# Optimization experiments

Measured on AMD Instinct MI355X. Metric: run time of the kernel, lower is better.

Reference implementation:

```python
import jax, jax.numpy as jnp
import numpy as np

NUM_HEADS = 4
NUM_GROUPS = 8
EPS = 1e-5


def group_norm(x, w, b):
    # x: [N, C, H, W], normalize over (C//G, H, W) per group
    N, C, H, W = x.shape
    xg = x.reshape(N, NUM_GROUPS, C // NUM_GROUPS, H, W)
    mu = jnp.mean(xg, axis=(2, 3, 4), keepdims=True)
    var = jnp.var(xg, axis=(2, 3, 4), keepdims=True)
    xn = ((xg - mu) * jax.lax.rsqrt(var + EPS)).reshape(N, C, H, W)
    return xn * w[None, :, None, None] + b[None, :, None, None]


def conv1x1(x, w, b):
    # x: [N, C, H, W], w: [Cout, Cin], b: [Cout]
    return jnp.einsum('nchw,dc->ndhw', x, w) + b[None, :, None, None]


def setup_inputs() -> dict:
    key = jax.random.key(0)
    ks = jax.random.split(key, 12)
    N, C, H, W = 2, 256, 64, 64
    s = 1.0 / np.sqrt(C)
    inp = {
        'x': jax.random.normal(ks[0], (N, C, H, W), jnp.float32),
        'mask': jax.random.randint(ks[1], (N, 1, H, W), 0, 2, jnp.int32),
        'norm_w': jnp.ones((C,), jnp.float32),
        'norm_b': jnp.zeros((C,), jnp.float32),
        'q_w': jax.random.normal(ks[2], (C, C), jnp.float32) * s,
        'q_b': jnp.zeros((C,), jnp.float32),
        'k_w': jax.random.normal(ks[3], (C, C), jnp.float32) * s,
        'k_b': jnp.zeros((C,), jnp.float32),
        'v_w': jax.random.normal(ks[4], (C, C), jnp.float32) * s,
        'v_b': jnp.zeros((C,), jnp.float32),
        'p_w': jax.random.normal(ks[5], (C, C), jnp.float32) * s,
        'p_b': jnp.zeros((C,), jnp.float32),
    }
    return inp


def reference(x, mask, norm_w, norm_b, q_w, q_b, k_w, k_b, v_w, v_b, p_w, p_b):
    N, C, H, W = x.shape
    hd = C // NUM_HEADS  # head dim
    L = H * W
    xn = group_norm(x, norm_w, norm_b)
    q = conv1x1(xn, q_w, q_b).reshape(N, NUM_HEADS, hd, L)
    k = conv1x1(xn, k_w, k_b).reshape(N, NUM_HEADS, hd, L)
    v = conv1x1(xn, v_w, v_b).reshape(N, NUM_HEADS, hd, L)
    scores = jnp.einsum('nhcl,nhck->nhlk', q, k) * (hd ** -0.5)
    probs = jax.nn.softmax(scores, axis=-1)
    out = jnp.einsum('nhlk,nhck->nhcl', probs, v).reshape(N, C, H, W)
    out = conv1x1(out, p_w, p_b)
    return (x + out, mask)
```

## Files before the change

kernel.cpp:

```cpp
#include <hip/hip_runtime.h>
#include <hip/hip_bf16.h>

#define NBATCH 2
#define CCH    256
#define LLEN   4096
#define NGROUP 8
#define CPG    32
#define NHEAD  4
#define HD     64
#define GEPS   1e-5f
#define QTILE  128
#define KTILE  64
#define KSPLIT 4
#define KEYS_PER_PART (LLEN / KSPLIT)
#define AITERS (KEYS_PER_PART / KTILE)
#define QSCALE 0.18033688011112042f
#define RS 264

typedef short bf16x8 __attribute__((ext_vector_type(8)));
typedef float f32x4  __attribute__((ext_vector_type(4)));

__device__ __forceinline__ unsigned short f2b(float f) {
  unsigned u = __float_as_uint(f);
  u += 0x7FFFu + ((u >> 16) & 1u);
  return (unsigned short)(u >> 16);
}
__device__ __forceinline__ unsigned pack2bf(float a, float b) {
  __hip_bfloat162 h = __float22bfloat162_rn(make_float2(a, b));
  union { __hip_bfloat162 h; unsigned u; } c;
  c.h = h;
  return c.u;
}
__device__ __forceinline__ float b2f(unsigned short h) {
  return __uint_as_float(((unsigned int)h) << 16);
}
__device__ __forceinline__ float exp2_(float x) {
#if __has_builtin(__builtin_amdgcn_exp2f)
  return __builtin_amdgcn_exp2f(x);
#else
  return exp2f(x);
#endif
}

__global__ __launch_bounds__(256) void setup_kernel(
    const float* __restrict__ qw, const float* __restrict__ kw,
    const float* __restrict__ vw, const float* __restrict__ pw,
    const float* __restrict__ qb, const float* __restrict__ kb,
    const float* __restrict__ vb, const float* __restrict__ pb,
    const float* __restrict__ x, const int* __restrict__ mask,
    unsigned short* __restrict__ w16, float* __restrict__ bias_ws,
    float* __restrict__ part, float* __restrict__ out2) {
  __shared__ float rs[4], rss[4];
  const int b = blockIdx.x;
  const int t = threadIdx.x;
  if (b < 256) {
    const int idx = b * 256 + t;
    const int m = idx >> 14;
    const float* src[4] = {qw, kw, vw, pw};
    const float sc = (m == 0) ? QSCALE : 1.0f;
    const float4 v = ((const float4*)src[m])[idx & 16383];
    ushort4 o;
    o.x = f2b(v.x * sc); o.y = f2b(v.y * sc);
    o.z = f2b(v.z * sc); o.w = f2b(v.w * sc);
    ((ushort4*)w16)[idx] = o;
    if (b == 0) {
      bias_ws[t]       = qb[t] * QSCALE;
      bias_ws[256 + t] = kb[t];
      bias_ws[512 + t] = vb[t];
      bias_ws[768 + t] = pb[t];
    }
  } else if (b < 384) {
    const int sb = b - 256;
    const int gidx = sb >> 3, sub = sb & 7;
    const float4* xp = (const float4*)(x + (size_t)gidx * (CPG * LLEN)) + (size_t)sub * 4096;
    float s = 0.f, ss = 0.f;
    for (int i = t; i < 4096; i += 256) {
      const float4 v = xp[i];
      s += v.x + v.y + v.z + v.w;
      ss = fmaf(v.x, v.x, ss);
      ss = fmaf(v.y, v.y, ss);
      ss = fmaf(v.z, v.z, ss);
      ss = fmaf(v.w, v.w, ss);
    }
#pragma unroll
    for (int off = 32; off; off >>= 1) {
      s  += __shfl_down(s, off);
      ss += __shfl_down(ss, off);
    }
    if ((t & 63) == 0) { rs[t >> 6] = s; rss[t >> 6] = ss; }
    __syncthreads();
    if (t == 0) {
      part[sb * 2 + 0] = rs[0] + rs[1] + rs[2] + rs[3];
      part[sb * 2 + 1] = rss[0] + rss[1] + rss[2] + rss[3];
    }
  } else {
    const int i = (b - 384) * 256 + t;
    out2[i] = (float)mask[i];
  }
}

__global__ __launch_bounds__(256) void gn_apply_kernel(const float* __restrict__ x,
                                                       const float* __restrict__ w,
                                                       const float* __restrict__ b,
                                                       const float* __restrict__ part,
                                                       unsigned short* __restrict__ xn16) {
  const int l0 = blockIdx.x * 32, c0 = blockIdx.y * 32, n = blockIdx.z;
  const int g16 = n * 8 + (c0 >> 5);
  float s = 0.f, ss = 0.f;
#pragma unroll
  for (int i = 0; i < 8; i++) {
    s  += part[(g16 * 8 + i) * 2 + 0];
    ss += part[(g16 * 8 + i) * 2 + 1];
  }
  const float inv_cnt = 1.0f / (float)(CPG * LLEN);
  const float mu = s * inv_cnt;
  const float rsg = rsqrtf(ss * inv_cnt - mu * mu + GEPS);
  __shared__ float tile[32][33];
  const int tx = threadIdx.x & 31, ty = threadIdx.x >> 5;
#pragma unroll
  for (int i = 0; i < 4; i++) {
    const int c = c0 + ty + 8 * i;
    const float wc = w[c], bc = b[c];
    const float v = x[((size_t)n * CCH + c) * LLEN + l0 + tx];
    tile[ty + 8 * i][tx] = (v - mu) * rsg * wc + bc;
  }
  __syncthreads();
#pragma unroll
  for (int i = 0; i < 4; i++) {
    const int l = l0 + ty + 8 * i;
    xn16[((size_t)n * LLEN + l) * CCH + c0 + tx] = f2b(tile[tx][ty + 8 * i]);
  }
}

__global__ __launch_bounds__(256, 2) void qkv_mfma_kernel(
    const unsigned short* __restrict__ xn16,
    const unsigned short* __restrict__ w16,
    const float* __restrict__ bias_ws,
    unsigned short* __restrict__ q16,
    unsigned short* __restrict__ k16,
    unsigned short* __restrict__ v16) {
  __shared__ __align__(16) unsigned short aS[64][RS];
  __shared__ __align__(16) unsigned short wS[64][RS];
  const int t = threadIdx.x;
  const int lane = t & 63, wv = t >> 6;
  const int col = lane & 15, quad = lane >> 4;
  const int m0 = blockIdx.x * 64;
  const int co0 = blockIdx.y * 64;
  const int wsel = blockIdx.z;

  {
    const int r = t >> 2, cu = (t & 3) * 64;
    const unsigned short* srcA = xn16 + (size_t)(m0 + r) * CCH + cu;
    const unsigned short* srcW = w16 + (size_t)wsel * (CCH * CCH) + (size_t)(co0 + r) * CCH + cu;
#pragma unroll
    for (int i = 0; i < 8; i++)
      *(uint4*)&aS[r][cu + i * 8] = *(const uint4*)(srcA + i * 8);
#pragma unroll
    for (int i = 0; i < 8; i++)
      *(uint4*)&wS[r][cu + i * 8] = *(const uint4*)(srcW + i * 8);
  }
  __syncthreads();

  f32x4 acc[4];
#pragma unroll
  for (int i = 0; i < 4; i++) acc[i] = {0.f, 0.f, 0.f, 0.f};

  if (wsel < 2) {
#pragma unroll
    for (int kc = 0; kc < 8; kc++) {
      const bf16x8 bw = *(const bf16x8*)&wS[wv * 16 + col][kc * 32 + quad * 8];
#pragma unroll
      for (int mt = 0; mt < 4; mt++) {
        const bf16x8 ax = *(const bf16x8*)&aS[mt * 16 + col][kc * 32 + quad * 8];
        acc[mt] = __builtin_amdgcn_mfma_f32_16x16x32_bf16(ax, bw, acc[mt], 0, 0, 0);
      }
    }
    unsigned short* dst = (wsel == 0) ? q16 : k16;
    const float bias = bias_ws[wsel * CCH + co0 + wv * 16 + col];
#pragma unroll
    for (int mt = 0; mt < 4; mt++)
#pragma unroll
      for (int r = 0; r < 4; r++)
        dst[(size_t)(m0 + mt * 16 + quad * 4 + r) * CCH + co0 + wv * 16 + col] =
            f2b(acc[mt][r] + bias);
  } else {
#pragma unroll
    for (int kc = 0; kc < 8; kc++) {
      const bf16x8 aw = *(const bf16x8*)&wS[wv * 16 + col][kc * 32 + quad * 8];
#pragma unroll
      for (int ct = 0; ct < 4; ct++) {
        const bf16x8 bx = *(const bf16x8*)&aS[ct * 16 + col][kc * 32 + quad * 8];
        acc[ct] = __builtin_amdgcn_mfma_f32_16x16x32_bf16(aw, bx, acc[ct], 0, 0, 0);
      }
    }
    const int n = m0 >> 12, l0 = m0 & 4095;
#pragma unroll
    for (int ct = 0; ct < 4; ct++)
#pragma unroll
      for (int r = 0; r < 4; r++) {
        const int cout = co0 + wv * 16 + quad * 4 + r;
        v16[((size_t)(n * CCH + cout)) * LLEN + l0 + ct * 16 + col] =
            f2b(acc[ct][r] + bias_ws[2 * CCH + cout]);
      }
  }
}

__global__ __launch_bounds__(256, 4) void attn_mfma_kernel(
    const unsigned short* __restrict__ q16,
    const unsigned short* __restrict__ k16,
    const unsigned short* __restrict__ v16,
    unsigned short* __restrict__ opA,
    unsigned short* __restrict__ opB,
    float* __restrict__ lpart) {
  __shared__ __align__(16) unsigned short kT[64][72];
  __shared__ __align__(16) unsigned short vT[64][72];
  __shared__ __align__(16) unsigned short pT[4][32][72];
  const int t = threadIdx.x;
  const int lane = t & 63, wv = t >> 6;
  const int col = lane & 15, quad = lane >> 4;
  const int q0 = blockIdx.x * QTILE;
  const int n = blockIdx.y >> 2, h = blockIdx.y & 3;
  const int part = blockIdx.z;
  const int hc = h * HD;
  const size_t baseNL = (size_t)n * LLEN;
  const int m_base = q0 + wv * 32;

  bf16x8 bq[2][2];
#pragma unroll
  for (int mt = 0; mt < 2; mt++) {
    const unsigned short* qr = q16 + (baseNL + m_base + mt * 16 + col) * CCH + hc + quad * 8;
    bq[mt][0] = *(const bf16x8*)qr;
    bq[mt][1] = *(const bf16x8*)(qr + 32);
  }
  bf16x8 bones;
#pragma unroll
  for (int i = 0; i < 8; i++) bones[i] = (short)0x3F80;

  f32x4 o[2][4], lacc[2];
#pragma unroll
  for (int mt = 0; mt < 2; mt++) {
    lacc[mt] = {0.f, 0.f, 0.f, 0.f};
#pragma unroll
    for (int ct = 0; ct < 4; ct++) o[mt][ct] = {0.f, 0.f, 0.f, 0.f};
  }

  const int srow = t >> 3;
  const int scol = (t & 7) * 8;
  const unsigned short* kgp = k16 + (baseNL + srow) * CCH + hc + scol;
  const unsigned short* vgp = v16 + ((size_t)(n * CCH + hc + srow)) * LLEN + scol;
  const size_t krstep = (size_t)32 * CCH;
  const size_t vrstep = (size_t)32 * LLEN;

  int kt = part * KEYS_PER_PART;
  uint4 rk0 = *(const uint4*)(kgp + (size_t)kt * CCH);
  uint4 rk1 = *(const uint4*)(kgp + (size_t)kt * CCH + krstep);
  uint4 rv0 = *(const uint4*)(vgp + kt);
  uint4 rv1 = *(const uint4*)(vgp + kt + vrstep);

  for (int it = 0; it < AITERS; it++) {
    __syncthreads();
    *(uint4*)&kT[srow][scol]      = rk0;
    *(uint4*)&kT[srow + 32][scol] = rk1;
    *(uint4*)&vT[srow][scol]      = rv0;
    *(uint4*)&vT[srow + 32][scol] = rv1;
    const int ktn = (it + 1 < AITERS) ? kt + KTILE : kt;
    rk0 = *(const uint4*)(kgp + (size_t)ktn * CCH);
    rk1 = *(const uint4*)(kgp + (size_t)ktn * CCH + krstep);
    rv0 = *(const uint4*)(vgp + ktn);
    rv1 = *(const uint4*)(vgp + ktn + vrstep);
    __syncthreads();

#pragma unroll
    for (int nt = 0; nt < 4; nt++) {
      const bf16x8 a0 = *(const bf16x8*)&kT[nt * 16 + col][quad * 8];
      const bf16x8 a1 = *(const bf16x8*)&kT[nt * 16 + col][32 + quad * 8];
#pragma unroll
      for (int mt = 0; mt < 2; mt++) {
        f32x4 s = {0.f, 0.f, 0.f, 0.f};
        s = __builtin_amdgcn_mfma_f32_16x16x32_bf16(a0, bq[mt][0], s, 0, 0, 0);
        s = __builtin_amdgcn_mfma_f32_16x16x32_bf16(a1, bq[mt][1], s, 0, 0, 0);
        const float p0 = exp2_(s[0]);
        const float p1 = exp2_(s[1]);
        const float p2 = exp2_(s[2]);
        const float p3 = exp2_(s[3]);
        uint2 w;
        w.x = pack2bf(p0, p1);
        w.y = pack2bf(p2, p3);
        *(uint2*)&pT[wv][mt * 16 + col][nt * 16 + quad * 4] = w;
      }
    }
    bf16x8 pa[2][2];
#pragma unroll
    for (int mt = 0; mt < 2; mt++) {
      pa[mt][0] = *(const bf16x8*)&pT[wv][mt * 16 + col][quad * 8];
      pa[mt][1] = *(const bf16x8*)&pT[wv][mt * 16 + col][32 + quad * 8];
      lacc[mt] = __builtin_amdgcn_mfma_f32_16x16x32_bf16(pa[mt][0], bones, lacc[mt], 0, 0, 0);
      lacc[mt] = __builtin_amdgcn_mfma_f32_16x16x32_bf16(pa[mt][1], bones, lacc[mt], 0, 0, 0);
    }
#pragma unroll
    for (int ct = 0; ct < 4; ct++) {
      const bf16x8 b0 = *(const bf16x8*)&vT[ct * 16 + col][quad * 8];
      const bf16x8 b1 = *(const bf16x8*)&vT[ct * 16 + col][32 + quad * 8];
#pragma unroll
      for (int mt = 0; mt < 2; mt++) {
        o[mt][ct] = __builtin_amdgcn_mfma_f32_16x16x32_bf16(pa[mt][0], b0, o[mt][ct], 0, 0, 0);
        o[mt][ct] = __builtin_amdgcn_mfma_f32_16x16x32_bf16(pa[mt][1], b1, o[mt][ct], 0, 0, 0);
      }
    }
    kt = ktn;
  }

  if (col == 0) {
#pragma unroll
    for (int mt = 0; mt < 2; mt++)
#pragma unroll
      for (int r = 0; r < 4; r++)
        lpart[((size_t)(part * NBATCH + n) * NHEAD + h) * LLEN +
              m_base + mt * 16 + quad * 4 + r] = lacc[mt][r];
  }
  const size_t TS = (size_t)NBATCH * LLEN * CCH;
  unsigned short* op = (part < 2) ? (opA + (size_t)part * TS) : (opB + (size_t)(part - 2) * TS);
#pragma unroll
  for (int mt = 0; mt < 2; mt++)
#pragma unroll
    for (int r = 0; r < 4; r++) {
      const size_t rowoff = (baseNL + m_base + mt * 16 + quad * 4 + r) * CCH + hc;
#pragma unroll
      for (int ct = 0; ct < 4; ct++)
        op[rowoff + ct * 16 + col] = f2b(o[mt][ct][r]);
    }
}

__global__ __launch_bounds__(256, 2) void proj_mfma_kernel(
    const unsigned short* __restrict__ opA,
    const unsigned short* __restrict__ opB,
    const float* __restrict__ lpart,
    const unsigned short* __restrict__ pw16,
    const float* __restrict__ pbias,
    const float* __restrict__ x,
    float* __restrict__ out) {
  __shared__ __align__(16) unsigned short aS[64][RS];
  __shared__ __align__(16) unsigned short wS[64][RS];
  const size_t TS = (size_t)NBATCH * LLEN * CCH;
  const size_t LPS = (size_t)NBATCH * NHEAD * LLEN;
  const int t = threadIdx.x;
  const int lane = t & 63, wv = t >> 6;
  const int col = lane & 15, quad = lane >> 4;
  const int m0 = blockIdx.x * 64;
  const int co0 = blockIdx.y * 64;
  const int n = m0 >> 12, l0 = m0 & 4095;

  {
    const int r = t >> 2, cu = (t & 3) * 64;
    const unsigned short* srcW = pw16 + (size_t)(co0 + r) * CCH + cu;
#pragma unroll
    for (int i = 0; i < 8; i++)
      *(uint4*)&wS[r][cu + i * 8] = *(const uint4*)(srcW + i * 8);
    const int l = l0 + r;
    const int h = t & 3;
    float ls = 0.f;
#pragma unroll
    for (int p = 0; p < 4; p++)
      ls += lpart[p * LPS + ((size_t)n * NHEAD + h) * LLEN + l];
    const float linv = 1.0f / ls;
    const size_t e0 = (size_t)(m0 + r) * CCH + cu;
#pragma unroll
    for (int i = 0; i < 8; i++) {
      const size_t e = e0 + (size_t)i * 8;
      const uint4 u0 = *(const uint4*)(opA + e);
      const uint4 u1 = *(const uint4*)(opA + TS + e);
      const uint4 u2 = *(const uint4*)(opB + e);
      const uint4 u3 = *(const uint4*)(opB + TS + e);
      uint4 res;
#pragma unroll
      for (int j = 0; j < 4; j++) {
        const unsigned a = (&u0.x)[j], bb = (&u1.x)[j], cc = (&u2.x)[j], dd = (&u3.x)[j];
        const float lo = (b2f((unsigned short)a) + b2f((unsigned short)bb) +
                          b2f((unsigned short)cc) + b2f((unsigned short)dd)) * linv;
        const float hi = (b2f((unsigned short)(a >> 16)) + b2f((unsigned short)(bb >> 16)) +
                          b2f((unsigned short)(cc >> 16)) + b2f((unsigned short)(dd >> 16))) * linv;
        (&res.x)[j] = pack2bf(lo, hi);
      }
      *(uint4*)&aS[r][cu + i * 8] = res;
    }
  }
  __syncthreads();

  f32x4 acc[4];
#pragma unroll
  for (int i = 0; i < 4; i++) acc[i] = {0.f, 0.f, 0.f, 0.f};
#pragma unroll
  for (int kc = 0; kc < 8; kc++) {
    const bf16x8 aw = *(const bf16x8*)&wS[wv * 16 + col][kc * 32 + quad * 8];
#pragma unroll
    for (int ct = 0; ct < 4; ct++) {
      const bf16x8 ba = *(const bf16x8*)&aS[ct * 16 + col][kc * 32 + quad * 8];
      acc[ct] = __builtin_amdgcn_mfma_f32_16x16x32_bf16(aw, ba, acc[ct], 0, 0, 0);
    }
  }
#pragma unroll
  for (int ct = 0; ct < 4; ct++)
#pragma unroll
    for (int r = 0; r < 4; r++) {
      const int cout = co0 + wv * 16 + quad * 4 + r;
      const size_t idx = ((size_t)(n * CCH + cout)) * LLEN + l0 + ct * 16 + col;
      out[idx] = acc[ct][r] + pbias[cout] + x[idx];
    }
}

extern "C" void kernel_launch(void* const* d_in, const int* in_sizes, int n_in,
                              void* d_out, int out_size, void* d_ws, size_t ws_size,
                              hipStream_t stream) {
  (void)in_sizes; (void)n_in; (void)out_size; (void)ws_size;
  const float* x      = (const float*)d_in[0];
  const int*   mask   = (const int*)d_in[1];
  const float* norm_w = (const float*)d_in[2];
  const float* norm_b = (const float*)d_in[3];
  const float* q_w    = (const float*)d_in[4];
  const float* q_b    = (const float*)d_in[5];
  const float* k_w    = (const float*)d_in[6];
  const float* k_b    = (const float*)d_in[7];
  const float* v_w    = (const float*)d_in[8];
  const float* v_b    = (const float*)d_in[9];
  const float* p_w    = (const float*)d_in[10];
  const float* p_b    = (const float*)d_in[11];

  const size_t TSZ = (size_t)NBATCH * LLEN * CCH;
  unsigned short* xn16 = (unsigned short*)d_ws;
  unsigned short* q16  = xn16 + TSZ;
  unsigned short* k16  = q16 + TSZ;
  unsigned short* v16  = k16 + TSZ;
  unsigned short* opA  = v16 + TSZ;
  unsigned short* opB  = opA + 2 * TSZ;
  unsigned short* w16  = opB + 2 * TSZ;
  float* bias_ws = (float*)(w16 + 4 * 65536);
  float* lpart   = bias_ws + 1024;
  float* part    = lpart + (size_t)KSPLIT * NBATCH * NHEAD * LLEN;

  float* out  = (float*)d_out;
  float* out2 = out + TSZ;

  setup_kernel<<<416, 256, 0, stream>>>(q_w, k_w, v_w, p_w, q_b, k_b, v_b, p_b,
                                        x, mask, w16, bias_ws, part, out2);
  gn_apply_kernel<<<dim3(LLEN / 32, CCH / 32, NBATCH), 256, 0, stream>>>(
      x, norm_w, norm_b, part, xn16);
  qkv_mfma_kernel<<<dim3((NBATCH * LLEN) / 64, CCH / 64, 3), 256, 0, stream>>>(
      xn16, w16, bias_ws, q16, k16, v16);
  attn_mfma_kernel<<<dim3(LLEN / QTILE, NBATCH * NHEAD, KSPLIT), 256, 0, stream>>>(
      q16, k16, v16, opA, opB, lpart);
  proj_mfma_kernel<<<dim3((NBATCH * LLEN) / 64, CCH / 64), 256, 0, stream>>>(
      opA, opB, lpart, w16 + 3 * 65536, bias_ws + 768, x, out);
}
```

Before: 167.4 us.

## Pre-swizzle Q/K/V into MFMA fragment layout and split keys across waves

```diff
diff --git a/kernel.cpp b/kernel.cpp
--- a/kernel.cpp
+++ b/kernel.cpp
@@ -9,11 +9,7 @@
 #define NHEAD  4
 #define HD     64
 #define GEPS   1e-5f
-#define QTILE  128
-#define KTILE  64
 #define KSPLIT 4
-#define KEYS_PER_PART (LLEN / KSPLIT)
-#define AITERS (KEYS_PER_PART / KTILE)
 #define QSCALE 0.18033688011112042f
 #define RS 264
 
@@ -165,6 +161,10 @@
 #pragma unroll
   for (int i = 0; i < 4; i++) acc[i] = {0.f, 0.f, 0.f, 0.f};
 
+  const int n = m0 >> 12;
+  const int h = co0 >> 6;
+  const size_t nh = (size_t)(n * NHEAD + h);
+
   if (wsel < 2) {
 #pragma unroll
     for (int kc = 0; kc < 8; kc++) {
@@ -177,12 +177,17 @@
     }
     unsigned short* dst = (wsel == 0) ? q16 : k16;
     const float bias = bias_ws[wsel * CCH + co0 + wv * 16 + col];
-#pragma unroll
-    for (int mt = 0; mt < 4; mt++)
+    const int ks = wv >> 1;
+    const int quadp = ((wv & 1) << 1) + (col >> 3);
+    const int j = col & 7;
+    const int t16b = (m0 & 4095) >> 4;
+#pragma unroll
+    for (int mt = 0; mt < 4; mt++) {
+      const size_t base = ((nh * 256 + (size_t)(t16b + mt)) * 2 + ks) * 512 + quadp * 128 + j;
 #pragma unroll
       for (int r = 0; r < 4; r++)
-        dst[(size_t)(m0 + mt * 16 + quad * 4 + r) * CCH + co0 + wv * 16 + col] =
-            f2b(acc[mt][r] + bias);
+        dst[base + (quad * 4 + r) * 8] = f2b(acc[mt][r] + bias);
+    }
   } else {
 #pragma unroll
     for (int kc = 0; kc < 8; kc++) {
@@ -193,142 +198,128 @@
         acc[ct] = __builtin_amdgcn_mfma_f32_16x16x32_bf16(aw, bx, acc[ct], 0, 0, 0);
       }
     }
-    const int n = m0 >> 12, l0 = m0 & 4095;
-#pragma unroll
-    for (int ct = 0; ct < 4; ct++)
+    const int kc32b = (m0 & 4095) >> 5;
+    const int j = col & 7;
+#pragma unroll
+    for (int ct = 0; ct < 4; ct++) {
+      const int kc32 = kc32b + (ct >> 1);
+      const int quadpp = ((ct & 1) << 1) + (col >> 3);
+      const size_t base = ((nh * 128 + (size_t)kc32) * 4 + wv) * 512 + quadpp * 128 + j;
 #pragma unroll
       for (int r = 0; r < 4; r++) {
-        const int cout = co0 + wv * 16 + quad * 4 + r;
-        v16[((size_t)(n * CCH + cout)) * LLEN + l0 + ct * 16 + col] =
-            f2b(acc[ct][r] + bias_ws[2 * CCH + cout]);
+        const float bias = bias_ws[2 * CCH + co0 + wv * 16 + quad * 4 + r];
+        v16[base + (quad * 4 + r) * 8] = f2b(acc[ct][r] + bias);
       }
-  }
-}
-
-__global__ __launch_bounds__(256, 4) void attn_mfma_kernel(
+    }
+  }
+}
+
+__global__ __launch_bounds__(256, 3) void attn_mfma_kernel(
     const unsigned short* __restrict__ q16,
     const unsigned short* __restrict__ k16,
     const unsigned short* __restrict__ v16,
     unsigned short* __restrict__ opA,
     unsigned short* __restrict__ opB,
     float* __restrict__ lpart) {
-  __shared__ __align__(16) unsigned short kT[64][72];
-  __shared__ __align__(16) unsigned short vT[64][72];
-  __shared__ __align__(16) unsigned short pT[4][32][72];
+  __shared__ __align__(16) unsigned char shraw[20480];
+  unsigned short (*pT)[64][40] = (unsigned short (*)[64][40])shraw;
+  f32x4 (*red)[4][64] = (f32x4 (*)[4][64])shraw;
+  f32x4 (*lred)[64] = (f32x4 (*)[64])(shraw + 16384);
   const int t = threadIdx.x;
   const int lane = t & 63, wv = t >> 6;
   const int col = lane & 15, quad = lane >> 4;
-  const int q0 = blockIdx.x * QTILE;
+  const int q0 = blockIdx.x * 64;
   const int n = blockIdx.y >> 2, h = blockIdx.y & 3;
   const int part = blockIdx.z;
   const int hc = h * HD;
   const size_t baseNL = (size_t)n * LLEN;
-  const int m_base = q0 + wv * 32;
-
-  bf16x8 bq[2][2];
-#pragma unroll
-  for (int mt = 0; mt < 2; mt++) {
-    const unsigned short* qr = q16 + (baseNL + m_base + mt * 16 + col) * CCH + hc + quad * 8;
-    bq[mt][0] = *(const bf16x8*)qr;
-    bq[mt][1] = *(const bf16x8*)(qr + 32);
-  }
+  const size_t nh = (size_t)(n * NHEAD + h);
+  const unsigned short* kb = k16 + nh * 262144;
+  const unsigned short* vb = v16 + nh * 262144;
+  const unsigned short* qb = q16 + nh * 262144;
+
+  bf16x8 bq[4][2];
+#pragma unroll
+  for (int qt = 0; qt < 4; qt++)
+#pragma unroll
+    for (int ks = 0; ks < 2; ks++)
+      bq[qt][ks] = *(const bf16x8*)(qb + (((size_t)((q0 >> 4) + qt) * 2 + ks) * 512) + lane * 8);
+
   bf16x8 bones;
 #pragma unroll
   for (int i = 0; i < 8; i++) bones[i] = (short)0x3F80;
 
-  f32x4 o[2][4], lacc[2];
-#pragma unroll
-  for (int mt = 0; mt < 2; mt++) {
-    lacc[mt] = {0.f, 0.f, 0.f, 0.f};
-#pragma unroll
-    for (int ct = 0; ct < 4; ct++) o[mt][ct] = {0.f, 0.f, 0.f, 0.f};
-  }
-
-  const int srow = t >> 3;
-  const int scol = (t & 7) * 8;
-  const unsigned short* kgp = k16 + (baseNL + srow) * CCH + hc + scol;
-  const unsigned short* vgp = v16 + ((size_t)(n * CCH + hc + srow)) * LLEN + scol;
-  const size_t krstep = (size_t)32 * CCH;
-  const size_t vrstep = (size_t)32 * LLEN;
-
-  int kt = part * KEYS_PER_PART;
-  uint4 rk0 = *(const uint4*)(kgp + (size_t)kt * CCH);
-  uint4 rk1 = *(const uint4*)(kgp + (size_t)kt * CCH + krstep);
-  uint4 rv0 = *(const uint4*)(vgp + kt);
-  uint4 rv1 = *(const uint4*)(vgp + kt + vrstep);
-
-  for (int it = 0; it < AITERS; it++) {
-    __syncthreads();
-    *(uint4*)&kT[srow][scol]      = rk0;
-    *(uint4*)&kT[srow + 32][scol] = rk1;
-    *(uint4*)&vT[srow][scol]      = rv0;
-    *(uint4*)&vT[srow + 32][scol] = rv1;
-    const int ktn = (it + 1 < AITERS) ? kt + KTILE : kt;
-    rk0 = *(const uint4*)(kgp + (size_t)ktn * CCH);
-    rk1 = *(const uint4*)(kgp + (size_t)ktn * CCH + krstep);
-    rv0 = *(const uint4*)(vgp + ktn);
-    rv1 = *(const uint4*)(vgp + ktn + vrstep);
-    __syncthreads();
-
-#pragma unroll
-    for (int nt = 0; nt < 4; nt++) {
-      const bf16x8 a0 = *(const bf16x8*)&kT[nt * 16 + col][quad * 8];
-      const bf16x8 a1 = *(const bf16x8*)&kT[nt * 16 + col][32 + quad * 8];
-#pragma unroll
-      for (int mt = 0; mt < 2; mt++) {
+  f32x4 o[4][4], lacc[4];
+#pragma unroll
+  for (int qt = 0; qt < 4; qt++) {
+    lacc[qt] = {0.f, 0.f, 0.f, 0.f};
+#pragma unroll
+    for (int ct = 0; ct < 4; ct++) o[qt][ct] = {0.f, 0.f, 0.f, 0.f};
+  }
+
+  const int kbase = part * 1024 + wv * 256;
+  for (int chunk = 0; chunk < 8; chunk++) {
+    const int kc = kbase + chunk * 32;
+    bf16x8 bv[4];
+#pragma unroll
+    for (int ct = 0; ct < 4; ct++)
+      bv[ct] = *(const bf16x8*)(vb + (((size_t)(kc >> 5) * 4 + ct) * 512) + lane * 8);
+    bf16x8 ka[2][2];
+#pragma unroll
+    for (int kt = 0; kt < 2; kt++)
+#pragma unroll
+      for (int ks = 0; ks < 2; ks++)
+        ka[kt][ks] = *(const bf16x8*)(kb + (((size_t)((kc >> 4) + kt) * 2 + ks) * 512) + lane * 8);
+
+#pragma unroll
+    for (int kt = 0; kt < 2; kt++)
+#pragma unroll
+      for (int qt = 0; qt < 4; qt++) {
         f32x4 s = {0.f, 0.f, 0.f, 0.f};
-        s = __builtin_amdgcn_mfma_f32_16x16x32_bf16(a0, bq[mt][0], s, 0, 0, 0);
-        s = __builtin_amdgcn_mfma_f32_16x16x32_bf16(a1, bq[mt][1], s, 0, 0, 0);
-        const float p0 = exp2_(s[0]);
-        const float p1 = exp2_(s[1]);
-        const float p2 = exp2_(s[2]);
-        const float p3 = exp2_(s[3]);
+        s = __builtin_amdgcn_mfma_f32_16x16x32_bf16(ka[kt][0], bq[qt][0], s, 0, 0, 0);
+        s = __builtin_amdgcn_mfma_f32_16x16x32_bf16(ka[kt][1], bq[qt][1], s, 0, 0, 0);
         uint2 w;
-        w.x = pack2bf(p0, p1);
-        w.y = pack2bf(p2, p3);
-        *(uint2*)&pT[wv][mt * 16 + col][nt * 16 + quad * 4] = w;
+        w.x = pack2bf(exp2_(s[0]), exp2_(s[1]));
+        w.y = pack2bf(exp2_(s[2]), exp2_(s[3]));
+        *(uint2*)&pT[wv][qt * 16 + col][kt * 16 + quad * 4] = w;
       }
-    }
-    bf16x8 pa[2][2];
-#pragma unroll
-    for (int mt = 0; mt < 2; mt++) {
-      pa[mt][0] = *(const bf16x8*)&pT[wv][mt * 16 + col][quad * 8];
-      pa[mt][1] = *(const bf16x8*)&pT[wv][mt * 16 + col][32 + quad * 8];
-      lacc[mt] = __builtin_amdgcn_mfma_f32_16x16x32_bf16(pa[mt][0], bones, lacc[mt], 0, 0, 0);
-      lacc[mt] = __builtin_amdgcn_mfma_f32_16x16x32_bf16(pa[mt][1], bones, lacc[mt], 0, 0, 0);
-    }
-#pragma unroll
-    for (int ct = 0; ct < 4; ct++) {
-      const bf16x8 b0 = *(const bf16x8*)&vT[ct * 16 + col][quad * 8];
-      const bf16x8 b1 = *(const bf16x8*)&vT[ct * 16 + col][32 + quad * 8];
-#pragma unroll
-      for (int mt = 0; mt < 2; mt++) {
-        o[mt][ct] = __builtin_amdgcn_mfma_f32_16x16x32_bf16(pa[mt][0], b0, o[mt][ct], 0, 0, 0);
-        o[mt][ct] = __builtin_amdgcn_mfma_f32_16x16x32_bf16(pa[mt][1], b1, o[mt][ct], 0, 0, 0);
-      }
-    }
-    kt = ktn;
-  }
-
-  if (col == 0) {
-#pragma unroll
-    for (int mt = 0; mt < 2; mt++)
-#pragma unroll
-      for (int r = 0; r < 4; r++)
-        lpart[((size_t)(part * NBATCH + n) * NHEAD + h) * LLEN +
-              m_base + mt * 16 + quad * 4 + r] = lacc[mt][r];
-  }
+#pragma unroll
+    for (int qt = 0; qt < 4; qt++) {
+      const bf16x8 pa = *(const bf16x8*)&pT[wv][qt * 16 + col][quad * 8];
+      lacc[qt] = __builtin_amdgcn_mfma_f32_16x16x32_bf16(pa, bones, lacc[qt], 0, 0, 0);
+#pragma unroll
+      for (int ct = 0; ct < 4; ct++)
+        o[qt][ct] = __builtin_amdgcn_mfma_f32_16x16x32_bf16(pa, bv[ct], o[qt][ct], 0, 0, 0);
+    }
+  }
+
   const size_t TS = (size_t)NBATCH * LLEN * CCH;
   unsigned short* op = (part < 2) ? (opA + (size_t)part * TS) : (opB + (size_t)(part - 2) * TS);
-#pragma unroll
-  for (int mt = 0; mt < 2; mt++)
-#pragma unroll
-    for (int r = 0; r < 4; r++) {
-      const size_t rowoff = (baseNL + m_base + mt * 16 + quad * 4 + r) * CCH + hc;
-#pragma unroll
-      for (int ct = 0; ct < 4; ct++)
-        op[rowoff + ct * 16 + col] = f2b(o[mt][ct][r]);
-    }
+  const size_t lbase = ((size_t)(part * NBATCH + n) * NHEAD + h) * LLEN;
+#pragma unroll
+  for (int qt = 0; qt < 4; qt++) {
+    __syncthreads();
+#pragma unroll
+    for (int ct = 0; ct < 4; ct++) red[wv][ct][lane] = o[qt][ct];
+    lred[wv][lane] = lacc[qt];
+    __syncthreads();
+    f32x4 os = red[0][wv][lane];
+    os += red[1][wv][lane];
+    os += red[2][wv][lane];
+    os += red[3][wv][lane];
+    f32x4 ls = lred[0][lane];
+    ls += lred[1][lane];
+    ls += lred[2][lane];
+    ls += lred[3][lane];
+#pragma unroll
+    for (int r = 0; r < 4; r++)
+      op[(baseNL + q0 + qt * 16 + quad * 4 + r) * CCH + hc + wv * 16 + col] = f2b(os[r]);
+    if (wv == 0 && col == 0) {
+#pragma unroll
+      for (int r = 0; r < 4; r++)
+        lpart[lbase + q0 + qt * 16 + quad * 4 + r] = ls[r];
+    }
+  }
 }
 
 __global__ __launch_bounds__(256, 2) void proj_mfma_kernel(
@@ -446,7 +437,7 @@
       x, norm_w, norm_b, part, xn16);
   qkv_mfma_kernel<<<dim3((NBATCH * LLEN) / 64, CCH / 64, 3), 256, 0, stream>>>(
       xn16, w16, bias_ws, q16, k16, v16);
-  attn_mfma_kernel<<<dim3(LLEN / QTILE, NBATCH * NHEAD, KSPLIT), 256, 0, stream>>>(
+  attn_mfma_kernel<<<dim3(LLEN / 64, NBATCH * NHEAD, KSPLIT), 256, 0, stream>>>(
       q16, k16, v16, opA, opB, lpart);
   proj_mfma_kernel<<<dim3((NBATCH * LLEN) / 64, CCH / 64), 256, 0, stream>>>(
       opA, opB, lpart, w16 + 3 * 65536, bias_ws + 768, x, out);
```

New measurement: 167.9 us. Within noise of the previous version (+0.3%).
